# Kernel tuning notes

Measured on AMD Instinct MI355X. Metric: run time of the kernel, lower is better.

Reference implementation:

```python
import jax, jax.numpy as jnp
import numpy as np

B, LQ, LK = 4, 512, 512
QF, KF, H, VD = 256, 256, 128, 256


def setup_inputs() -> dict:
    key = jax.random.key(0)
    ks = jax.random.split(key, 7)
    queries = jax.random.normal(ks[0], (B, LQ, QF), dtype=jnp.float32)
    keys = jax.random.normal(ks[1], (B, LK, KF), dtype=jnp.float32)
    values = jax.random.normal(ks[2], (B, LK, VD), dtype=jnp.float32)
    valid_lens = jax.random.randint(ks[3], (B,), 1, LK + 1)  # at least 1 valid key
    # nn.Linear weights (torch layout: [out_features, in_features]), Kaiming-uniform-ish scale
    W_q = jax.random.normal(ks[4], (H, QF), dtype=jnp.float32) / np.sqrt(QF).astype(np.float32)
    W_k = jax.random.normal(ks[5], (H, KF), dtype=jnp.float32) / np.sqrt(KF).astype(np.float32)
    W_v = jax.random.normal(ks[6], (H,), dtype=jnp.float32) / np.sqrt(H).astype(np.float32)
    return {"queries": queries, "keys": keys, "values": values,
            "valid_lens": valid_lens, "W_q": W_q, "W_k": W_k, "W_v": W_v}


def reference(queries, keys, values, valid_lens, W_q, W_k, W_v):
    # Projections: a(q,k) = W_v^T tanh(W_q q + W_k k)
    q = jnp.einsum('bqf,hf->bqh', queries, W_q)   # [B,LQ,H]
    k = jnp.einsum('bkf,hf->bkh', keys, W_k)      # [B,LK,H]
    feats = jnp.tanh(q[:, :, None, :] + k[:, None, :, :])  # [B,LQ,LK,H]
    scores = jnp.einsum('bqkh,h->bqk', feats, W_v)          # [B,LQ,LK]
    # masked softmax over key axis: positions >= valid_len get -1e9
    key_pos = jnp.arange(scores.shape[-1])[None, None, :]   # [1,1,LK]
    mask = key_pos < valid_lens[:, None, None]               # [B,1,LK] broadcasts over LQ
    scores = jnp.where(mask, scores, jnp.float32(-1e9))
    attn = jax.nn.softmax(scores, axis=-1)                   # [B,LQ,LK]
    # dropout p=0.0 (eval) -> identity
    out = jnp.einsum('bqk,bkv->bqv', attn, values)           # [B,LQ,VD]
    return out, attn
```

## Files before the change

### kernel.cpp

```cpp
#include <hip/hip_runtime.h>
#include <cstddef>

#define NB 4
#define LQ 512
#define LK 512
#define QF 256
#define NH 128
#define VD 256

__device__ __forceinline__ float fexp2(float x) {
    float r; asm("v_exp_f32 %0, %1" : "=v"(r) : "v"(x)); return r;
}
__device__ __forceinline__ float frcp(float x) {
    float r; asm("v_rcp_f32 %0, %1" : "=v"(r) : "v"(x)); return r;
}
__device__ __forceinline__ void fma4(float4& acc, float s, const float4 v) {
    acc.x = __builtin_fmaf(s, v.x, acc.x);
    acc.y = __builtin_fmaf(s, v.y, acc.y);
    acc.z = __builtin_fmaf(s, v.z, acc.z);
    acc.w = __builtin_fmaf(s, v.w, acc.w);
}

constexpr float kLog2e    = 1.4426950408889634f;
constexpr float kPreScale = 2.0f * kLog2e;

__global__ __launch_bounds__(256) void transw_kernel(
    const float* __restrict__ W_q, const float* __restrict__ W_k,
    float4* __restrict__ wt)
{
    const int bid = blockIdx.x;
    const int mat = bid & 1;
    const int f4b = (bid >> 1) * 8;
    const float4* W4 = (const float4*)(mat ? W_k : W_q);
    float4* o = wt + (size_t)mat * 64 * NH;

    const int t  = threadIdx.x;
    const int h  = t & 127;
    const int fo = t >> 7;
    #pragma unroll
    for (int it = 0; it < 4; ++it) {
        const int f4 = f4b + fo + 2 * it;
        o[f4 * NH + h] = W4[h * 64 + f4];
    }
}

__global__ __launch_bounds__(256) void proj_kernel(
    const float* __restrict__ queries, const float* __restrict__ keys,
    const float4* __restrict__ wt,
    float* __restrict__ eq, float* __restrict__ ekt4f)
{
    const int bid   = blockIdx.x;
    const int which = bid & 1;
    const int rt    = bid >> 1;
    const int row0  = rt * 8;
    const float4* In4 = (const float4*)(which ? keys : queries);
    const float4* w4  = wt + (size_t)which * 64 * NH;

    __shared__ float4 rows[8][64];

    const int t    = threadIdx.x;
    const int lane = t & 63;
    const int wid  = t >> 6;

    {
        const int f4 = t & 63;
        const int r  = t >> 6;
        rows[r][f4]     = In4[(size_t)(row0 + r) * 64 + f4];
        rows[r + 4][f4] = In4[(size_t)(row0 + r + 4) * 64 + f4];
    }
    __syncthreads();

    const int r0 = wid * 2;
    float acc[2][2] = {};
    #pragma unroll 4
    for (int f4 = 0; f4 < 64; ++f4) {
        const float4 w0 = w4[f4 * NH + lane];
        const float4 w1 = w4[f4 * NH + lane + 64];
        #pragma unroll
        for (int r = 0; r < 2; ++r) {
            const float4 x = rows[r0 + r][f4];
            acc[r][0] += w0.x * x.x + w0.y * x.y + w0.z * x.z + w0.w * x.w;
            acc[r][1] += w1.x * x.x + w1.y * x.y + w1.z * x.z + w1.w * x.w;
        }
    }

    if (which == 0) {
        #pragma unroll
        for (int r = 0; r < 2; ++r) {
            const size_t o = (size_t)(row0 + r0 + r) * NH;
            eq[o + lane]      = fexp2(kPreScale * acc[r][0]);
            eq[o + lane + 64] = fexp2(kPreScale * acc[r][1]);
        }
    } else {
        const int b  = row0 >> 9;
        const int j0 = (row0 & 511) + r0;
        #pragma unroll
        for (int r = 0; r < 2; ++r) {
            #pragma unroll
            for (int s = 0; s < 2; ++s) {
                const int h = lane + 64 * s;
                ekt4f[(((size_t)b * 32 + (h >> 2)) * LK + j0 + r) * 4 + (h & 3)]
                    = fexp2(kPreScale * acc[r][s]);
            }
        }
    }
}

__global__ __launch_bounds__(1024, 8) void fused_kernel(
    const float* __restrict__ eq, const float* __restrict__ ekt4f,
    const float* __restrict__ values, const int* __restrict__ valid_lens,
    const float* __restrict__ W_v,
    float* __restrict__ out, float* __restrict__ attn_out)
{
    const int id = blockIdx.x;
    const int b  = id & 3;
    const int i0 = (id >> 2) * 4;
    const int vl = valid_lens[b];

    __shared__ float  eq_lds[4][NH];
    __shared__ float  wv[NH];
    __shared__ float  attn_t[LK][4];
    __shared__ float4 pacc[8][4][VD / 4];
    __shared__ float  reds[16];

    const int t    = threadIdx.x;
    const int wid  = t >> 6;
    const int lane = t & 63;
    const int qi   = wid & 3;
    const int g    = wid >> 2;

    if (t < 4 * NH) ((float*)eq_lds)[t] = eq[(size_t)(b * LQ + i0) * NH + t];
    if (t < NH)     wv[t] = W_v[t];
    __syncthreads();

    const float4* q4  = (const float4*)eq_lds[qi];
    const float4* wv4 = (const float4*)wv;

    float sumA = 0.f, sumW = 0.f;
    #pragma unroll 8
    for (int h4 = 0; h4 < NH / 4; ++h4) {
        const float4 w = wv4[h4];
        sumW += (w.x + w.y) + (w.z + w.w);
        sumA += (fabsf(w.x) + fabsf(w.y)) + (fabsf(w.z) + fabsf(w.w));
    }

    float p[2];
    float sum = 0.f;
    #pragma unroll
    for (int u = 0; u < 2; ++u) {
        const int jj = g + 4 * u;
        const int j  = jj * 64 + lane;
        float pv = 0.f;
        if (jj * 64 < vl) {
            const float4* pk4 = (const float4*)ekt4f + (size_t)b * 32 * LK + j;
            float a0 = 0.f, a1 = 0.f, a2 = 0.f, a3 = 0.f;
            #pragma unroll 4
            for (int h4 = 0; h4 < NH / 4; ++h4) {
                const float4 e = pk4[(size_t)h4 * LK];
                const float4 w = wv4[h4];
                const float4 q = q4[h4];
                a0 = __builtin_fmaf(w.x, frcp(__builtin_fmaf(q.x, e.x, 1.f)), a0);
                a1 = __builtin_fmaf(w.y, frcp(__builtin_fmaf(q.y, e.y, 1.f)), a1);
                a2 = __builtin_fmaf(w.z, frcp(__builtin_fmaf(q.z, e.z, 1.f)), a2);
                a3 = __builtin_fmaf(w.w, frcp(__builtin_fmaf(q.w, e.w, 1.f)), a3);
            }
            const float s = __builtin_fmaf(-2.f, (a0 + a1) + (a2 + a3), sumW);
            pv = fexp2((s - sumA) * kLog2e);
            if (j >= vl) pv = 0.f;
        }
        p[u] = pv;
        sum += pv;
    }

    #pragma unroll
    for (int off = 1; off < 64; off <<= 1)
        sum += __shfl_xor(sum, off, 64);
    if (lane == 0) reds[wid] = sum;
    __syncthreads();
    const float rs = frcp((reds[qi] + reds[qi + 4]) + (reds[qi + 8] + reds[qi + 12]));

    float* arow = attn_out + (size_t)(b * LQ + i0 + qi) * LK;
    #pragma unroll
    for (int u = 0; u < 2; ++u) {
        const int j = (g + 4 * u) * 64 + lane;
        const float a = p[u] * rs;
        arow[j]       = a;
        attn_t[j][qi] = a;
    }
    __syncthreads();

    const int j0 = wid * 32;
    const int j1 = min(j0 + 32, vl);
    float4 acc4[4];
    #pragma unroll
    for (int q = 0; q < 4; ++q) acc4[q] = float4{0.f, 0.f, 0.f, 0.f};

    const float4* v4 = (const float4*)(values + (size_t)b * LK * VD);
    for (int j = j0; j < j1; ++j) {
        const float4 a  = *(const float4*)&attn_t[j][0];
        const float4 vv = v4[(size_t)j * 64 + lane];
        fma4(acc4[0], a.x, vv);
        fma4(acc4[1], a.y, vv);
        fma4(acc4[2], a.z, vv);
        fma4(acc4[3], a.w, vv);
    }

    if (wid < 8) {
        #pragma unroll
        for (int q = 0; q < 4; ++q) pacc[wid][q][lane] = acc4[q];
    }
    __syncthreads();
    if (wid >= 8) {
        #pragma unroll
        for (int q = 0; q < 4; ++q) {
            const float4 pv = pacc[wid - 8][q][lane];
            pacc[wid - 8][q][lane] =
                float4{pv.x + acc4[q].x, pv.y + acc4[q].y,
                       pv.z + acc4[q].z, pv.w + acc4[q].w};
        }
    }
    __syncthreads();

    {
        const int q = t >> 8;
        const int c = t & 255;
        float s = 0.f;
        #pragma unroll
        for (int k = 0; k < 8; ++k)
            s += ((const float*)&pacc[k][q][0])[c];
        out[(size_t)(b * LQ + i0 + q) * VD + c] = s;
    }
}

extern "C" void kernel_launch(void* const* d_in, const int* in_sizes, int n_in,
                              void* d_out, int out_size, void* d_ws, size_t ws_size,
                              hipStream_t stream)
{
    const float* queries    = (const float*)d_in[0];
    const float* keys       = (const float*)d_in[1];
    const float* values     = (const float*)d_in[2];
    const int*   valid_lens = (const int*)  d_in[3];
    const float* W_q        = (const float*)d_in[4];
    const float* W_k        = (const float*)d_in[5];
    const float* W_v        = (const float*)d_in[6];

    float* out      = (float*)d_out;
    float* attn_out = out + (size_t)NB * LQ * VD;

    float*  eq    = (float*)d_ws;
    float*  ekt4f = eq + (size_t)NB * LQ * NH;
    float4* wt    = (float4*)(ekt4f + (size_t)NB * NH * LK);

    transw_kernel<<<16,  256,  0, stream>>>(W_q, W_k, wt);
    proj_kernel  <<<512, 256,  0, stream>>>(queries, keys, wt, eq, ekt4f);
    fused_kernel <<<512, 1024, 0, stream>>>(eq, ekt4f, values, valid_lens, W_v,
                                            out, attn_out);
}
```

Measured before the change: 47.83 us.

## Process two query rows per block instead of four, doubling grid size

The fused attention kernel now assigns two query rows per 1024-thread block instead of four, so the grid grows to 1024 blocks and each thread computes one score instead of two. Blocks are ordered batch-major rather than interleaved across batches. This increases parallelism and shortens per-thread score work. In exchange, each block streams the value rows for only two queries, which doubles total reads of the values tensor and of the key features, and the final reduction leaves half the threads idle.

```diff
diff --git a/kernel.cpp b/kernel.cpp
--- a/kernel.cpp
+++ b/kernel.cpp
@@ -113,23 +113,23 @@
     float* __restrict__ out, float* __restrict__ attn_out)
 {
     const int id = blockIdx.x;
-    const int b  = id & 3;
-    const int i0 = (id >> 2) * 4;
+    const int b  = id >> 8;
+    const int i0 = (id & 255) * 2;
     const int vl = valid_lens[b];
 
-    __shared__ float  eq_lds[4][NH];
+    __shared__ float  eq_lds[2][NH];
     __shared__ float  wv[NH];
-    __shared__ float  attn_t[LK][4];
-    __shared__ float4 pacc[8][4][VD / 4];
+    __shared__ float  attn_t[LK][2];
+    __shared__ float4 pacc[8][2][VD / 4];
     __shared__ float  reds[16];
 
     const int t    = threadIdx.x;
     const int wid  = t >> 6;
     const int lane = t & 63;
-    const int qi   = wid & 3;
-    const int g    = wid >> 2;
-
-    if (t < 4 * NH) ((float*)eq_lds)[t] = eq[(size_t)(b * LQ + i0) * NH + t];
+    const int qi   = wid & 1;
+    const int g    = wid >> 1;
+
+    if (t < 2 * NH) ((float*)eq_lds)[t] = eq[(size_t)(b * LQ + i0) * NH + t];
     if (t < NH)     wv[t] = W_v[t];
     __syncthreads();
 
@@ -144,84 +144,72 @@
         sumA += (fabsf(w.x) + fabsf(w.y)) + (fabsf(w.z) + fabsf(w.w));
     }
 
-    float p[2];
-    float sum = 0.f;
-    #pragma unroll
-    for (int u = 0; u < 2; ++u) {
-        const int jj = g + 4 * u;
-        const int j  = jj * 64 + lane;
-        float pv = 0.f;
-        if (jj * 64 < vl) {
-            const float4* pk4 = (const float4*)ekt4f + (size_t)b * 32 * LK + j;
-            float a0 = 0.f, a1 = 0.f, a2 = 0.f, a3 = 0.f;
-            #pragma unroll 4
-            for (int h4 = 0; h4 < NH / 4; ++h4) {
-                const float4 e = pk4[(size_t)h4 * LK];
-                const float4 w = wv4[h4];
-                const float4 q = q4[h4];
-                a0 = __builtin_fmaf(w.x, frcp(__builtin_fmaf(q.x, e.x, 1.f)), a0);
-                a1 = __builtin_fmaf(w.y, frcp(__builtin_fmaf(q.y, e.y, 1.f)), a1);
-                a2 = __builtin_fmaf(w.z, frcp(__builtin_fmaf(q.z, e.z, 1.f)), a2);
-                a3 = __builtin_fmaf(w.w, frcp(__builtin_fmaf(q.w, e.w, 1.f)), a3);
-            }
-            const float s = __builtin_fmaf(-2.f, (a0 + a1) + (a2 + a3), sumW);
-            pv = fexp2((s - sumA) * kLog2e);
-            if (j >= vl) pv = 0.f;
-        }
-        p[u] = pv;
-        sum += pv;
-    }
-
+    const int j = g * 64 + lane;
+    float pv = 0.f;
+    if (g * 64 < vl) {
+        const float4* pk4 = (const float4*)ekt4f + (size_t)b * 32 * LK + j;
+        float a0 = 0.f, a1 = 0.f, a2 = 0.f, a3 = 0.f;
+        #pragma unroll 4
+        for (int h4 = 0; h4 < NH / 4; ++h4) {
+            const float4 e = pk4[(size_t)h4 * LK];
+            const float4 w = wv4[h4];
+            const float4 q = q4[h4];
+            a0 = __builtin_fmaf(w.x, frcp(__builtin_fmaf(q.x, e.x, 1.f)), a0);
+            a1 = __builtin_fmaf(w.y, frcp(__builtin_fmaf(q.y, e.y, 1.f)), a1);
+            a2 = __builtin_fmaf(w.z, frcp(__builtin_fmaf(q.z, e.z, 1.f)), a2);
+            a3 = __builtin_fmaf(w.w, frcp(__builtin_fmaf(q.w, e.w, 1.f)), a3);
+        }
+        const float s = __builtin_fmaf(-2.f, (a0 + a1) + (a2 + a3), sumW);
+        pv = fexp2((s - sumA) * kLog2e);
+        if (j >= vl) pv = 0.f;
+    }
+
+    float sum = pv;
     #pragma unroll
     for (int off = 1; off < 64; off <<= 1)
         sum += __shfl_xor(sum, off, 64);
     if (lane == 0) reds[wid] = sum;
     __syncthreads();
-    const float rs = frcp((reds[qi] + reds[qi + 4]) + (reds[qi + 8] + reds[qi + 12]));
-
-    float* arow = attn_out + (size_t)(b * LQ + i0 + qi) * LK;
+    float rsum = 0.f;
     #pragma unroll
-    for (int u = 0; u < 2; ++u) {
-        const int j = (g + 4 * u) * 64 + lane;
-        const float a = p[u] * rs;
-        arow[j]       = a;
+    for (int k = 0; k < 8; ++k) rsum += reds[qi + 2 * k];
+    const float rs = frcp(rsum);
+
+    {
+        const float a = pv * rs;
+        attn_out[(size_t)(b * LQ + i0 + qi) * LK + j] = a;
         attn_t[j][qi] = a;
     }
     __syncthreads();
 
+    float4 oacc[2] = {float4{0.f,0.f,0.f,0.f}, float4{0.f,0.f,0.f,0.f}};
     const int j0 = wid * 32;
     const int j1 = min(j0 + 32, vl);
-    float4 acc4[4];
-    #pragma unroll
-    for (int q = 0; q < 4; ++q) acc4[q] = float4{0.f, 0.f, 0.f, 0.f};
-
     const float4* v4 = (const float4*)(values + (size_t)b * LK * VD);
-    for (int j = j0; j < j1; ++j) {
-        const float4 a  = *(const float4*)&attn_t[j][0];
-        const float4 vv = v4[(size_t)j * 64 + lane];
-        fma4(acc4[0], a.x, vv);
-        fma4(acc4[1], a.y, vv);
-        fma4(acc4[2], a.z, vv);
-        fma4(acc4[3], a.w, vv);
+    for (int jj = j0; jj < j1; ++jj) {
+        const float2 a2 = *(const float2*)&attn_t[jj][0];
+        const float4 vv = v4[(size_t)jj * 64 + lane];
+        fma4(oacc[0], a2.x, vv);
+        fma4(oacc[1], a2.y, vv);
     }
 
     if (wid < 8) {
-        #pragma unroll
-        for (int q = 0; q < 4; ++q) pacc[wid][q][lane] = acc4[q];
+        pacc[wid][0][lane] = oacc[0];
+        pacc[wid][1][lane] = oacc[1];
     }
     __syncthreads();
     if (wid >= 8) {
         #pragma unroll
-        for (int q = 0; q < 4; ++q) {
-            const float4 pv = pacc[wid - 8][q][lane];
+        for (int q = 0; q < 2; ++q) {
+            const float4 p0 = pacc[wid - 8][q][lane];
             pacc[wid - 8][q][lane] =
-                float4{pv.x + acc4[q].x, pv.y + acc4[q].y,
-                       pv.z + acc4[q].z, pv.w + acc4[q].w};
-        }
-    }
-    __syncthreads();
-
-    {
+                float4{p0.x + oacc[q].x, p0.y + oacc[q].y,
+                       p0.z + oacc[q].z, p0.w + oacc[q].w};
+        }
+    }
+    __syncthreads();
+
+    if (t < 512) {
         const int q = t >> 8;
         const int c = t & 255;
         float s = 0.f;
@@ -251,8 +239,8 @@
     float*  ekt4f = eq + (size_t)NB * LQ * NH;
     float4* wt    = (float4*)(ekt4f + (size_t)NB * NH * LK);
 
-    transw_kernel<<<16,  256,  0, stream>>>(W_q, W_k, wt);
-    proj_kernel  <<<512, 256,  0, stream>>>(queries, keys, wt, eq, ekt4f);
-    fused_kernel <<<512, 1024, 0, stream>>>(eq, ekt4f, values, valid_lens, W_v,
-                                            out, attn_out);
-}
+    transw_kernel<<<16,   256,  0, stream>>>(W_q, W_k, wt);
+    proj_kernel  <<<512,  256,  0, stream>>>(queries, keys, wt, eq, ekt4f);
+    fused_kernel <<<1024, 1024, 0, stream>>>(eq, ekt4f, values, valid_lens, W_v,
+                                             out, attn_out);
+}
```

Measured after the change: 49.59 us. 3.7% more time.
